# Optimization experiments

Hardware: AMD Instinct MI355X
Metric: run time of the kernel (lower is better)

Reference implementation:

```python
import jax, jax.numpy as jnp
import numpy as np

B, T, U, V, H, KA, KO = 64, 600, 64, 80, 512, 10, 20


def setup_inputs() -> dict:
    key = jax.random.key(0)
    ks = jax.random.split(key, 12)
    std = 0.075
    p = lambda k, shape: jax.random.normal(k, shape, jnp.float32) * std
    return dict(
        char_seq=jax.random.randint(ks[0], (B, U), 0, V),
        char_mask=jnp.ones((B, U), jnp.float32),
        strokes=jax.random.normal(ks[1], (B, T, 3), jnp.float32),
        strokes_mask=jnp.ones((B, T), jnp.float32),
        lstm0_Wih=p(ks[2], (4 * H, 3 + V)), lstm0_Whh=p(ks[3], (4 * H, H)), lstm0_b=jnp.zeros((4 * H,), jnp.float32),
        win_W=p(ks[4], (3 * KA, H)), win_b=jnp.zeros((3 * KA,), jnp.float32),
        lstm1_Wih=p(ks[5], (4 * H, 3 + V + H)), lstm1_Whh=p(ks[6], (4 * H, H)), lstm1_b=jnp.zeros((4 * H,), jnp.float32),
        lstm2_Wih=p(ks[7], (4 * H, 3 + V + H)), lstm2_Whh=p(ks[8], (4 * H, H)), lstm2_b=jnp.zeros((4 * H,), jnp.float32),
        fc_W=p(ks[9], (6 * KO + 1, 3 * H)), fc_b=jnp.zeros((6 * KO + 1,), jnp.float32),
    )


def _lstm_cell(gates_x, h, c, Whh):
    # gates_x already contains x@Wih.T + b; PyTorch gate order: i, f, g, o
    gates = gates_x + h @ Whh.T
    i, f, g, o = jnp.split(gates, 4, axis=-1)
    c = jax.nn.sigmoid(f) * c + jax.nn.sigmoid(i) * jnp.tanh(g)
    h = jax.nn.sigmoid(o) * jnp.tanh(c)
    return h, c


def _run_lstm(x, Wih, Whh, b):
    # x: [B, T, F]; precompute input projection once (big GEMM), scan only on h.
    gx = jnp.einsum('btf,gf->btg', x, Wih) + b  # [B,T,4H]
    h0 = jnp.zeros((x.shape[0], H), x.dtype)
    c0 = jnp.zeros((x.shape[0], H), x.dtype)

    def step(carry, g_t):
        h, c = carry
        h, c = _lstm_cell(g_t, h, c, Whh)
        return (h, c), h

    _, hs = jax.lax.scan(step, (h0, c0), gx.transpose(1, 0, 2))
    return hs.transpose(1, 0, 2)  # [B,T,H]


def _forward(char_seq, char_mask, strokes,
             lstm0_Wih, lstm0_Whh, lstm0_b, win_W, win_b,
             lstm1_Wih, lstm1_Whh, lstm1_b, lstm2_Wih, lstm2_Whh, lstm2_b,
             fc_W, fc_b):
    char_oh = jax.nn.one_hot(char_seq, V, dtype=jnp.float32) * char_mask[..., None]  # [B,U,V]
    u_grid = jnp.arange(U, dtype=jnp.float32)  # char positions

    h0 = jnp.zeros((B, H), jnp.float32)
    c0 = jnp.zeros((B, H), jnp.float32)
    w0 = jnp.zeros((B, V), jnp.float32)
    k0 = jnp.zeros((B, KA), jnp.float32)

    def step(carry, x_t):
        h, c, w, k = carry
        inp = jnp.concatenate([x_t, w], axis=-1)  # [B, 3+V]
        gates = inp @ lstm0_Wih.T + lstm0_b
        h, c = _lstm_cell(gates, h, c, lstm0_Whh)
        # Gaussian attention window (Graves 2013)
        p = h @ win_W.T + win_b  # [B, 3K]
        alpha, beta, kap_hat = jnp.split(jnp.exp(p), 3, axis=-1)
        k = k + kap_hat  # [B,K]
        phi = jnp.sum(alpha[:, :, None] * jnp.exp(-beta[:, :, None] * (k[:, :, None] - u_grid) ** 2), axis=1)
        phi = phi * char_mask  # [B,U]
        w = jnp.einsum('bu,buv->bv', phi, char_oh)
        return (h, c, w, k), (h, w)

    _, (h_seq, w_seq) = jax.lax.scan(step, (h0, c0, w0, k0), strokes.transpose(1, 0, 2))
    lstm0_out = h_seq.transpose(1, 0, 2)   # [B,T,H]
    attn_out = w_seq.transpose(1, 0, 2)    # [B,T,V]

    lstm1_out = _run_lstm(jnp.concatenate([strokes, attn_out, lstm0_out], -1), lstm1_Wih, lstm1_Whh, lstm1_b)
    lstm2_out = _run_lstm(jnp.concatenate([strokes, attn_out, lstm1_out], -1), lstm2_Wih, lstm2_Whh, lstm2_b)

    final = jnp.einsum('bth,gh->btg', jnp.concatenate([lstm0_out, lstm1_out, lstm2_out], -1), fc_W) + fc_b
    # parse_outputs: split [2K, 2K, K, K, 1]
    myu = final[..., : 2 * KO]
    log_sigma = final[..., 2 * KO: 4 * KO]
    pi = final[..., 4 * KO: 5 * KO]
    rho = final[..., 5 * KO: 6 * KO]
    eos = final[..., 6 * KO:]
    log_pi = jax.nn.log_softmax(pi, axis=-1)
    rho = jnp.tanh(rho)
    eos = jax.nn.sigmoid(-eos)
    myu = myu.reshape(myu.shape[:-1] + (KO, 2))
    log_sigma = log_sigma.reshape(log_sigma.shape[:-1] + (KO, 2))
    return (log_pi, myu, log_sigma, rho, eos)


def reference(char_seq, char_mask, strokes, strokes_mask,
              lstm0_Wih, lstm0_Whh, lstm0_b, win_W, win_b,
              lstm1_Wih, lstm1_Whh, lstm1_b, lstm2_Wih, lstm2_Whh, lstm2_b,
              fc_W, fc_b):
    # strokes_mask is unused by forward() in the original module (only in losses)
    return _forward(char_seq, char_mask, strokes,
                    lstm0_Wih, lstm0_Whh, lstm0_b, win_W, win_b,
                    lstm1_Wih, lstm1_Whh, lstm1_b, lstm2_Wih, lstm2_Whh, lstm2_b,
                    fc_W, fc_b)
```

## Files before the change

kernel.cpp:

```cpp
#include <hip/hip_runtime.h>
#include <math.h>

#define B_ 64
#define T_ 600
#define U_ 64
#define V_ 80
#define H_ 512
#define KA_ 10
#define KO_ 20

#define S0_ 600
#define S12_ 1108
#define NLB_ 64
#define NWB_ 64

typedef unsigned u32x4 __attribute__((ext_vector_type(4)));

__device__ __forceinline__ float sigmf(float x){ return 1.0f/(1.0f+expf(-x)); }

__device__ __forceinline__ int coh_load_i32(const int* p){
    int v;
    asm volatile("global_load_dword %0, %1, off sc0 sc1\n\ts_waitcnt vmcnt(0)"
                 : "=v"(v) : "v"(p) : "memory");
    return v;
}
__device__ __forceinline__ void coh_store_u32(unsigned* p, unsigned v){
    asm volatile("global_store_dword %0, %1, off sc0 sc1" :: "v"(p), "v"(v) : "memory");
}
__device__ __forceinline__ void coh_store_u128(unsigned* p, u32x4 v){
    asm volatile("global_store_dwordx4 %0, %1, off sc0 sc1" :: "v"(p), "v"(v) : "memory");
}
__device__ __forceinline__ void spin_ge(int* p, int target){
    while (coh_load_i32(p) < target) __builtin_amdgcn_s_sleep(1);
}
#define BLOCK_WAIT(p, tgt) do { if (threadIdx.x == 0) spin_ge((p), (tgt)); __syncthreads(); } while (0)

__device__ __forceinline__ float blo(unsigned u){ return __uint_as_float(u << 16); }
__device__ __forceinline__ float bhi(unsigned u){ return __uint_as_float(u & 0xffff0000u); }
__device__ __forceinline__ unsigned pack_bf16(float a, float b){
    return ((__float_as_uint(a) + 0x8000u) >> 16) | ((__float_as_uint(b) + 0x8000u) & 0xffff0000u);
}

__global__ __launch_bounds__(64) void k_prep(
    const float* __restrict__ W0ih, const float* __restrict__ W0hh,
    const float* __restrict__ W1ih, const float* __restrict__ W1hh,
    const float* __restrict__ W2ih, const float* __restrict__ W2hh,
    float* __restrict__ wpad)
{
    int r = blockIdx.x;
    int tid = threadIdx.x;
    if (r < 2048){
        float* dst = wpad + (size_t)r*S0_;
        const float* sih = W0ih + (size_t)r*83;
        const float* shh = W0hh + (size_t)r*512;
        if (tid < 3) dst[tid] = sih[tid];
        if (tid == 3) dst[3] = 0.f;
        for (int v=tid; v<V_; v+=64) dst[4+v] = sih[3+v];
        for (int k=tid; k<H_; k+=64) dst[84+k] = shh[k];
    } else {
        int rr = r - 2048;
        int layer = rr >> 11;
        int row = rr & 2047;
        const float* sih = (layer==0 ? W1ih : W2ih) + (size_t)row*595;
        const float* shh = (layer==0 ? W1hh : W2hh) + (size_t)row*512;
        float* dst = wpad + (size_t)2048*S0_ + ((size_t)layer*2048 + row)*S12_;
        if (tid < 3) dst[tid] = sih[tid];
        if (tid == 3) dst[3] = 0.f;
        for (int v=tid; v<V_; v+=64) dst[4+v] = sih[3+v];
        for (int k=tid; k<H_; k+=64) dst[84+k] = sih[83+k];
        for (int k=tid; k<H_; k+=64) dst[596+k] = shh[k];
    }
}

#define FMA8(W, OFF) do { \
    float4 qa = *(const float4*)((W) + (OFF)); \
    float4 qb = *(const float4*)((W) + (OFF) + 4); \
    A0 += x0*qa.x + x1*qa.y + x2*qa.z + x3*qa.w + x4*qb.x + x5*qb.y + x6*qb.z + x7*qb.w; \
} while (0)

__global__ __launch_bounds__(512, 2) void k_pipe(
    const float* __restrict__ strokes,
    const int*   __restrict__ char_seq,
    const float* __restrict__ char_mask,
    const float* __restrict__ wpad,
    const float* __restrict__ winW, const float* __restrict__ winb,
    const float* __restrict__ b0, const float* __restrict__ b1, const float* __restrict__ b2,
    unsigned* __restrict__ out0b, unsigned* __restrict__ out1b, unsigned* __restrict__ out2b,
    unsigned* __restrict__ attnb, int* __restrict__ sync)
{
    __builtin_amdgcn_fence(__ATOMIC_ACQUIRE, "agent");

    int* c0 = sync;
    int* c1 = sync + 640;
    int* c2 = sync + 1280;
    int* cw = sync + 1920;

    const int bid = blockIdx.x;
    const int tid = threadIdx.x;
    const int b   = tid & 63;
    const int r   = tid >> 6;

    __shared__ float sh[8][64];
    __shared__ float shh[512];
    __shared__ float pp[30][16];
    __shared__ float sa[KA_], sbv[KA_], sk[KA_], skst[KA_];
    __shared__ float sphi[U_];
    __shared__ float satt[V_];
    __shared__ int   sseq[U_];
    __shared__ float smask[U_];

    if (bid >= 192){
        const int wb = bid - 192;
        if (tid < U_){ sseq[tid] = char_seq[wb*U_+tid]; smask[tid] = char_mask[wb*U_+tid]; }
        __syncthreads();
        for (int t=0; t<T_; ++t){
            BLOCK_WAIT(&c0[t], NLB_);
            if (tid < 64){
                uint4 q = ((const uint4*)out0b)[((size_t)t*64 + tid)*64 + wb];
                shh[8*tid+0]=blo(q.x); shh[8*tid+1]=bhi(q.x);
                shh[8*tid+2]=blo(q.y); shh[8*tid+3]=bhi(q.y);
                shh[8*tid+4]=blo(q.z); shh[8*tid+5]=bhi(q.z);
                shh[8*tid+6]=blo(q.w); shh[8*tid+7]=bhi(q.w);
            }
            __syncthreads();
            if (tid < 480){
                int rr = tid >> 4, p = tid & 15;
                const float* wrow = winW + (size_t)rr*H_;
                float acc = 0.f;
                #pragma unroll 8
                for (int i=0; i<32; ++i) acc += shh[p+16*i]*wrow[p+16*i];
                pp[rr][p] = acc;
            }
            __syncthreads();
            if (tid < 30){
                float pv = winb[tid];
                #pragma unroll
                for (int i=0; i<16; ++i) pv += pp[tid][i];
                float e = expf(pv);
                if (tid < KA_) sa[tid] = e;
                else if (tid < 2*KA_) sbv[tid-KA_] = e;
                else {
                    int a2 = tid - 2*KA_;
                    float kn = ((t == 0) ? 0.f : skst[a2]) + e;
                    skst[a2] = kn; sk[a2] = kn;
                }
            }
            __syncthreads();
            if (tid < U_){
                float acc = 0.f;
                #pragma unroll
                for (int a=0; a<KA_; ++a){
                    float d = sk[a] - (float)tid;
                    acc += sa[a]*expf(-sbv[a]*d*d);
                }
                sphi[tid] = acc * smask[tid]*smask[tid];
            }
            __syncthreads();
            if (tid < V_){
                float wv = 0.f;
                for (int u=0; u<U_; ++u) wv += (sseq[u] == tid) ? sphi[u] : 0.f;
                satt[tid] = wv;
            }
            __syncthreads();
            if (tid < 40){
                coh_store_u32(attnb + (size_t)t*2560 + (size_t)wb*40 + tid,
                              pack_bf16(satt[2*tid], satt[2*tid+1]));
                asm volatile("s_waitcnt vmcnt(0)" ::: "memory");
            }
            __syncthreads();
            if (tid == 0) atomicAdd(&cw[t], 1);
        }
        return;
    }

    const int l  = bid >> 6;
    const int ub = (bid & 63) * 8;
    const int cu = ub + r;

    const float* wbase; const float* bias_p; size_t wst;
    unsigned* hbo; const unsigned* hbp; int* cself; int* cprev;
    if (l == 0){ wbase = wpad;                                  wst = S0_;  bias_p = b0; hbo = out0b; hbp = nullptr; cself = c0; cprev = nullptr; }
    else if (l == 1){ wbase = wpad + (size_t)2048*S0_;          wst = S12_; bias_p = b1; hbo = out1b; hbp = out0b;  cself = c1; cprev = c0; }
    else { wbase = wpad + (size_t)2048*S0_ + (size_t)2048*S12_; wst = S12_; bias_p = b2; hbo = out2b; hbp = out1b;  cself = c2; cprev = c1; }

    const float* w0 = wbase + (size_t)(0*H_+cu)*wst;
    const float* w1 = wbase + (size_t)(1*H_+cu)*wst;
    const float* w2 = wbase + (size_t)(2*H_+cu)*wst;
    const float* w3 = wbase + (size_t)(3*H_+cu)*wst;

    const float bq0 = bias_p[0*H_+cu];
    const float bq1 = bias_p[1*H_+cu];
    const float bq2 = bias_p[2*H_+cu];
    const float bq3 = bias_p[3*H_+cu];
    float creg = 0.f;

    for (int t=0; t<T_; ++t){
        float a0, a1, a2, a3;
        {
            const float* sr = strokes + ((size_t)b*T_ + t)*3;
            float sx=sr[0], sy=sr[1], sz=sr[2];
            a0 = sx*w0[0] + sy*w0[1] + sz*w0[2];
            a1 = sx*w1[0] + sy*w1[1] + sz*w1[2];
            a2 = sx*w2[0] + sy*w2[1] + sz*w2[2];
            a3 = sx*w3[0] + sy*w3[1] + sz*w3[2];
        }

        if (l == 0){
            if (t > 0){
                BLOCK_WAIT(&c0[t-1], NLB_);
                const uint4* hp = (const uint4*)out0b + (size_t)(t-1)*4096 + b;
                #pragma unroll 4
                for (int kp=0; kp<64; ++kp){
                    uint4 q = hp[(size_t)kp*64];
                    float x0=blo(q.x),x1=bhi(q.x),x2=blo(q.y),x3=bhi(q.y);
                    float x4=blo(q.z),x5=bhi(q.z),x6=blo(q.w),x7=bhi(q.w);
                    int o = 84 + 8*kp;
                    { float A0=a0; FMA8(w0,o); a0=A0; }
                    { float A0=a1; FMA8(w1,o); a1=A0; }
                    { float A0=a2; FMA8(w2,o); a2=A0; }
                    { float A0=a3; FMA8(w3,o); a3=A0; }
                }
                BLOCK_WAIT(&cw[t-1], NWB_);
                const uint4* ap = (const uint4*)(attnb + (size_t)(t-1)*2560 + (size_t)b*40);
                #pragma unroll
                for (int j=0; j<10; ++j){
                    uint4 q = ap[j];
                    float x0=blo(q.x),x1=bhi(q.x),x2=blo(q.y),x3=bhi(q.y);
                    float x4=blo(q.z),x5=bhi(q.z),x6=blo(q.w),x7=bhi(q.w);
                    int o = 4 + 8*j;
                    { float A0=a0; FMA8(w0,o); a0=A0; }
                    { float A0=a1; FMA8(w1,o); a1=A0; }
                    { float A0=a2; FMA8(w2,o); a2=A0; }
                    { float A0=a3; FMA8(w3,o); a3=A0; }
                }
            }
        } else {
            if (tid == 0){
                if (t > 0) spin_ge(&cself[t-1], NLB_);
                spin_ge(&cprev[t], NLB_);
                spin_ge(&cw[t], NWB_);
            }
            __syncthreads();
            const uint4* hc = (const uint4*)hbp + (size_t)t*4096 + b;
            if (t > 0){
                const uint4* ho = (const uint4*)hbo + (size_t)(t-1)*4096 + b;
                #pragma unroll 2
                for (int kp=0; kp<64; ++kp){
                    uint4 qo = ho[(size_t)kp*64];
                    uint4 qc = hc[(size_t)kp*64];
                    {
                        float x0=blo(qo.x),x1=bhi(qo.x),x2=blo(qo.y),x3=bhi(qo.y);
                        float x4=blo(qo.z),x5=bhi(qo.z),x6=blo(qo.w),x7=bhi(qo.w);
                        int o = 596 + 8*kp;
                        { float A0=a0; FMA8(w0,o); a0=A0; }
                        { float A0=a1; FMA8(w1,o); a1=A0; }
                        { float A0=a2; FMA8(w2,o); a2=A0; }
                        { float A0=a3; FMA8(w3,o); a3=A0; }
                    }
                    {
                        float x0=blo(qc.x),x1=bhi(qc.x),x2=blo(qc.y),x3=bhi(qc.y);
                        float x4=blo(qc.z),x5=bhi(qc.z),x6=blo(qc.w),x7=bhi(qc.w);
                        int o = 84 + 8*kp;
                        { float A0=a0; FMA8(w0,o); a0=A0; }
                        { float A0=a1; FMA8(w1,o); a1=A0; }
                        { float A0=a2; FMA8(w2,o); a2=A0; }
                        { float A0=a3; FMA8(w3,o); a3=A0; }
                    }
                }
            } else {
                #pragma unroll 4
                for (int kp=0; kp<64; ++kp){
                    uint4 qc = hc[(size_t)kp*64];
                    float x0=blo(qc.x),x1=bhi(qc.x),x2=blo(qc.y),x3=bhi(qc.y);
                    float x4=blo(qc.z),x5=bhi(qc.z),x6=blo(qc.w),x7=bhi(qc.w);
                    int o = 84 + 8*kp;
                    { float A0=a0; FMA8(w0,o); a0=A0; }
                    { float A0=a1; FMA8(w1,o); a1=A0; }
                    { float A0=a2; FMA8(w2,o); a2=A0; }
                    { float A0=a3; FMA8(w3,o); a3=A0; }
                }
            }
            const uint4* ap = (const uint4*)(attnb + (size_t)t*2560 + (size_t)b*40);
            #pragma unroll
            for (int j=0; j<10; ++j){
                uint4 q = ap[j];
                float x0=blo(q.x),x1=bhi(q.x),x2=blo(q.y),x3=bhi(q.y);
                float x4=blo(q.z),x5=bhi(q.z),x6=blo(q.w),x7=bhi(q.w);
                int o = 4 + 8*j;
                { float A0=a0; FMA8(w0,o); a0=A0; }
                { float A0=a1; FMA8(w1,o); a1=A0; }
                { float A0=a2; FMA8(w2,o); a2=A0; }
                { float A0=a3; FMA8(w3,o); a3=A0; }
            }
        }

        {
            float gi  = a0 + bq0;
            float gf  = a1 + bq1;
            float gg_ = a2 + bq2;
            float go  = a3 + bq3;
            float cold = (t == 0) ? 0.f : creg;
            float cnew = sigmf(gf)*cold + sigmf(gi)*tanhf(gg_);
            creg = cnew;
            sh[r][b] = sigmf(go)*tanhf(cnew);
        }
        __syncthreads();
        if (tid < 64){
            u32x4 v;
            v.x = pack_bf16(sh[0][tid], sh[1][tid]);
            v.y = pack_bf16(sh[2][tid], sh[3][tid]);
            v.z = pack_bf16(sh[4][tid], sh[5][tid]);
            v.w = pack_bf16(sh[6][tid], sh[7][tid]);
            coh_store_u128(hbo + (size_t)t*16384 + (size_t)(ub>>3)*256 + tid*4, v);
            asm volatile("s_waitcnt vmcnt(0)" ::: "memory");
        }
        __syncthreads();
        if (tid == 0) atomicAdd(&cself[t], 1);
    }
}

__global__ __launch_bounds__(256) void k_fc(
    const unsigned* __restrict__ out0b, const unsigned* __restrict__ out1b, const unsigned* __restrict__ out2b,
    const float* __restrict__ fcW, const float* __restrict__ fcb, float* __restrict__ out)
{
    int t = blockIdx.x; int tid = threadIdx.x;
    int b = tid & 63; int gq = tid >> 6;
    __shared__ float smraw[128*65];

    float acc[31];
    #pragma unroll
    for (int i=0; i<31; ++i) acc[i] = 0.f;

    const unsigned* hbs[3] = {out0b, out1b, out2b};
    for (int seg=0; seg<3; ++seg){
        const uint4* o = (const uint4*)hbs[seg];
        for (int kc=0; kc<H_; kc+=128){
            int kp0 = kc >> 3;
            __syncthreads();
            #pragma unroll
            for (int rr=0; rr<4; ++rr){
                int idx = tid + 256*rr;
                int kq  = idx >> 6;
                int bb  = idx & 63;
                uint4 v = o[((size_t)t*64 + kp0 + kq)*64 + bb];
                int kb = kq*8;
                smraw[(kb+0)*65+bb]=blo(v.x); smraw[(kb+1)*65+bb]=bhi(v.x);
                smraw[(kb+2)*65+bb]=blo(v.y); smraw[(kb+3)*65+bb]=bhi(v.y);
                smraw[(kb+4)*65+bb]=blo(v.z); smraw[(kb+5)*65+bb]=bhi(v.z);
                smraw[(kb+6)*65+bb]=blo(v.w); smraw[(kb+7)*65+bb]=bhi(v.w);
            }
            __syncthreads();
            for (int kk=0; kk<128; kk+=4){
                float a0 = smraw[(kk+0)*65+b];
                float a1 = smraw[(kk+1)*65+b];
                float a2 = smraw[(kk+2)*65+b];
                float a3 = smraw[(kk+3)*65+b];
                int K = seg*H_ + kc + kk;
                #pragma unroll
                for (int i=0; i<30; ++i){
                    float4 w = *(const float4*)(fcW + (size_t)(gq+4*i)*1536 + K);
                    acc[i] += a0*w.x + a1*w.y + a2*w.z + a3*w.w;
                }
                if (gq == 0){
                    float4 w = *(const float4*)(fcW + (size_t)120*1536 + K);
                    acc[30] += a0*w.x + a1*w.y + a2*w.z + a3*w.w;
                }
            }
        }
    }
    __syncthreads();
    #pragma unroll
    for (int i=0; i<30; ++i) smraw[(gq+4*i)*64 + b] = acc[i] + fcb[gq+4*i];
    if (gq == 0) smraw[120*64 + b] = acc[30] + fcb[120];
    __syncthreads();

    if (tid < 64){
        size_t bt = (size_t)b*T_ + t;
        float* myu = out + 768000;
        #pragma unroll
        for (int q=0; q<10; ++q){
            float4 v;
            v.x = smraw[(4*q+0)*64+b]; v.y = smraw[(4*q+1)*64+b];
            v.z = smraw[(4*q+2)*64+b]; v.w = smraw[(4*q+3)*64+b];
            *(float4*)(myu + bt*40 + 4*q) = v;
        }
        float* lsg = out + 2304000;
        #pragma unroll
        for (int q=0; q<10; ++q){
            float4 v;
            v.x = smraw[(40+4*q+0)*64+b]; v.y = smraw[(40+4*q+1)*64+b];
            v.z = smraw[(40+4*q+2)*64+b]; v.w = smraw[(40+4*q+3)*64+b];
            *(float4*)(lsg + bt*40 + 4*q) = v;
        }
        float pi[KO_];
        float m = -1e30f;
        #pragma unroll
        for (int ko=0; ko<KO_; ++ko){ pi[ko] = smraw[(80+ko)*64+b]; m = fmaxf(m, pi[ko]); }
        float s = 0.f;
        #pragma unroll
        for (int ko=0; ko<KO_; ++ko) s += expf(pi[ko]-m);
        float lse = m + logf(s);
        #pragma unroll
        for (int q=0; q<5; ++q){
            float4 v;
            v.x = pi[4*q+0]-lse; v.y = pi[4*q+1]-lse; v.z = pi[4*q+2]-lse; v.w = pi[4*q+3]-lse;
            *(float4*)(out + bt*20 + 4*q) = v;
        }
        float* rho = out + 3840000;
        #pragma unroll
        for (int q=0; q<5; ++q){
            float4 v;
            v.x = tanhf(smraw[(100+4*q+0)*64+b]); v.y = tanhf(smraw[(100+4*q+1)*64+b]);
            v.z = tanhf(smraw[(100+4*q+2)*64+b]); v.w = tanhf(smraw[(100+4*q+3)*64+b]);
            *(float4*)(rho + bt*20 + 4*q) = v;
        }
        out[4608000 + bt] = 1.f/(1.f + expf(smraw[120*64+b]));
    }
}

extern "C" void kernel_launch(void* const* d_in, const int* in_sizes, int n_in,
                              void* d_out, int out_size, void* d_ws, size_t ws_size,
                              hipStream_t stream)
{
    const int*   char_seq  = (const int*)  d_in[0];
    const float* char_mask = (const float*)d_in[1];
    const float* strokes   = (const float*)d_in[2];
    const float* W0ih = (const float*)d_in[4];
    const float* W0hh = (const float*)d_in[5];
    const float* b0   = (const float*)d_in[6];
    const float* winW = (const float*)d_in[7];
    const float* winb = (const float*)d_in[8];
    const float* W1ih = (const float*)d_in[9];
    const float* W1hh = (const float*)d_in[10];
    const float* b1   = (const float*)d_in[11];
    const float* W2ih = (const float*)d_in[12];
    const float* W2hh = (const float*)d_in[13];
    const float* b2   = (const float*)d_in[14];
    const float* fcW  = (const float*)d_in[15];
    const float* fcb  = (const float*)d_in[16];

    unsigned* out0b = (unsigned*)d_ws;
    unsigned* out1b = out0b + 9830400;
    unsigned* out2b = out1b + 9830400;
    unsigned* attnb = out2b + 9830400;
    float*    wpad  = (float*)(attnb + 1536000);
    int*      sync  = (int*)(wpad + 5767168);

    (void)hipMemsetAsync(sync, 0, 2560*sizeof(int), stream);

    hipLaunchKernelGGL(k_prep, dim3(6144), dim3(64), 0, stream,
        W0ih, W0hh, W1ih, W1hh, W2ih, W2hh, wpad);

    hipLaunchKernelGGL(k_pipe, dim3(256), dim3(512), 0, stream,
        strokes, char_seq, char_mask, wpad, winW, winb, b0, b1, b2,
        out0b, out1b, out2b, attnb, sync);

    hipLaunchKernelGGL(k_fc, dim3(600), dim3(256), 0, stream,
        out0b, out1b, out2b, fcW, fcb, (float*)d_out);
}
```

Before: 54.57 ms.

## Keep fp16 LSTM weights resident in LDS, use fdot2, replace atomic counters with per-block flags

Recurrent and input weights are packed to fp16 in the prep kernel. Each persistent block loads its 32 gate rows into dynamic shared memory once and reuses them for all 600 steps, instead of streaming fp32 weights from global or L2 every step. Dot products use the packed fp16 dot instruction, and the activations are exchanged as fp16 rather than bf16. Cross-block synchronisation switches from atomicAdd counters to per-block padded flags that 64 threads poll in parallel. This cuts per-step memory traffic and atomic latency, at the cost of fp16 precision and about 71KB of LDS per block, which may limit occupancy.

```diff
diff --git a/kernel.cpp b/kernel.cpp
--- a/kernel.cpp
+++ b/kernel.cpp
@@ -9,99 +9,124 @@
 #define KA_ 10
 #define KO_ 20
 
-#define S0_ 600
-#define S12_ 1108
-#define NLB_ 64
-#define NWB_ 64
+#define RW0   300
+#define RW12  556
+#define WOFF1 614400
+#define WOFF2 1753088
+#define WOFFW 2891776
+#define FSTRIDE 16
 
 typedef unsigned u32x4 __attribute__((ext_vector_type(4)));
+typedef _Float16 h2_t __attribute__((ext_vector_type(2)));
 
 __device__ __forceinline__ float sigmf(float x){ return 1.0f/(1.0f+expf(-x)); }
 
-__device__ __forceinline__ int coh_load_i32(const int* p){
-    int v;
+static __device__ __forceinline__ h2_t bch(unsigned u){ return __builtin_bit_cast(h2_t, u); }
+static __device__ __forceinline__ unsigned pkh(float a, float b){
+    return __builtin_bit_cast(unsigned, __builtin_amdgcn_cvt_pkrtz(a, b));
+}
+static __device__ __forceinline__ float hlo(unsigned u){ return (float)bch(u)[0]; }
+static __device__ __forceinline__ float hhi(unsigned u){ return (float)bch(u)[1]; }
+
+#if __has_builtin(__builtin_amdgcn_fdot2)
+static __device__ __forceinline__ float fd2(unsigned a, unsigned b, float c){
+    return __builtin_amdgcn_fdot2(bch(a), bch(b), c, false);
+}
+#else
+static __device__ __forceinline__ float fd2(unsigned a, unsigned b, float c){
+    return c + hlo(a)*hlo(b) + hhi(a)*hhi(b);
+}
+#endif
+
+static __device__ __forceinline__ float dot8(uint4 q, uint4 w, float acc){
+    acc = fd2(q.x, w.x, acc);
+    acc = fd2(q.y, w.y, acc);
+    acc = fd2(q.z, w.z, acc);
+    acc = fd2(q.w, w.w, acc);
+    return acc;
+}
+
+static __device__ __forceinline__ unsigned coh_load_u32(const unsigned* p){
+    unsigned v;
     asm volatile("global_load_dword %0, %1, off sc0 sc1\n\ts_waitcnt vmcnt(0)"
                  : "=v"(v) : "v"(p) : "memory");
     return v;
 }
-__device__ __forceinline__ void coh_store_u32(unsigned* p, unsigned v){
+static __device__ __forceinline__ void coh_store_u32(unsigned* p, unsigned v){
     asm volatile("global_store_dword %0, %1, off sc0 sc1" :: "v"(p), "v"(v) : "memory");
 }
-__device__ __forceinline__ void coh_store_u128(unsigned* p, u32x4 v){
+static __device__ __forceinline__ void coh_store_u128(unsigned* p, u32x4 v){
     asm volatile("global_store_dwordx4 %0, %1, off sc0 sc1" :: "v"(p), "v"(v) : "memory");
 }
-__device__ __forceinline__ void spin_ge(int* p, int target){
-    while (coh_load_i32(p) < target) __builtin_amdgcn_s_sleep(1);
-}
-#define BLOCK_WAIT(p, tgt) do { if (threadIdx.x == 0) spin_ge((p), (tgt)); __syncthreads(); } while (0)
-
-__device__ __forceinline__ float blo(unsigned u){ return __uint_as_float(u << 16); }
-__device__ __forceinline__ float bhi(unsigned u){ return __uint_as_float(u & 0xffff0000u); }
-__device__ __forceinline__ unsigned pack_bf16(float a, float b){
-    return ((__float_as_uint(a) + 0x8000u) >> 16) | ((__float_as_uint(b) + 0x8000u) & 0xffff0000u);
+static __device__ __forceinline__ void wait_role(const unsigned* f){
+    if (threadIdx.x < 64){
+        const unsigned* p = f + threadIdx.x*FSTRIDE;
+        while (coh_load_u32(p) == 0){}
+    }
+    __syncthreads();
 }
 
 __global__ __launch_bounds__(64) void k_prep(
     const float* __restrict__ W0ih, const float* __restrict__ W0hh,
     const float* __restrict__ W1ih, const float* __restrict__ W1hh,
     const float* __restrict__ W2ih, const float* __restrict__ W2hh,
-    float* __restrict__ wpad)
+    const float* __restrict__ winW,
+    unsigned* __restrict__ wpad32)
 {
-    int r = blockIdx.x;
-    int tid = threadIdx.x;
-    if (r < 2048){
-        float* dst = wpad + (size_t)r*S0_;
-        const float* sih = W0ih + (size_t)r*83;
-        const float* shh = W0hh + (size_t)r*512;
-        if (tid < 3) dst[tid] = sih[tid];
-        if (tid == 3) dst[3] = 0.f;
-        for (int v=tid; v<V_; v+=64) dst[4+v] = sih[3+v];
-        for (int k=tid; k<H_; k+=64) dst[84+k] = shh[k];
+    int r = blockIdx.x; int tid = threadIdx.x;
+    if (r < 6144){
+        int layer = r >> 11;
+        int row = r & 2047;
+        const float* ih; const float* hh; unsigned* dst; int RW;
+        if (layer == 0){ ih = W0ih + (size_t)row*83;  hh = W0hh + (size_t)row*512; dst = wpad32 + (size_t)row*RW0;           RW = RW0; }
+        else if (layer == 1){ ih = W1ih + (size_t)row*595; hh = W1hh + (size_t)row*512; dst = wpad32 + WOFF1 + (size_t)row*RW12; RW = RW12; }
+        else { ih = W2ih + (size_t)row*595; hh = W2hh + (size_t)row*512; dst = wpad32 + WOFF2 + (size_t)row*RW12; RW = RW12; }
+        for (int j = tid; j < RW; j += 64){
+            float f[2];
+            #pragma unroll
+            for (int q = 0; q < 2; ++q){
+                int e = 2*j + q;
+                float v = 0.f;
+                if (e < 3) v = ih[e];
+                else if (e >= 8 && e < 88) v = ih[3 + e - 8];
+                else if (e >= 88 && e < 600) v = (layer == 0) ? hh[e-88] : ih[83 + e - 88];
+                else if (e >= 600 && e < 1112 && layer != 0) v = hh[e-600];
+                f[q] = v;
+            }
+            dst[j] = pkh(f[0], f[1]);
+        }
     } else {
-        int rr = r - 2048;
-        int layer = rr >> 11;
-        int row = rr & 2047;
-        const float* sih = (layer==0 ? W1ih : W2ih) + (size_t)row*595;
-        const float* shh = (layer==0 ? W1hh : W2hh) + (size_t)row*512;
-        float* dst = wpad + (size_t)2048*S0_ + ((size_t)layer*2048 + row)*S12_;
-        if (tid < 3) dst[tid] = sih[tid];
-        if (tid == 3) dst[3] = 0.f;
-        for (int v=tid; v<V_; v+=64) dst[4+v] = sih[3+v];
-        for (int k=tid; k<H_; k+=64) dst[84+k] = sih[83+k];
-        for (int k=tid; k<H_; k+=64) dst[596+k] = shh[k];
-    }
-}
-
-#define FMA8(W, OFF) do { \
-    float4 qa = *(const float4*)((W) + (OFF)); \
-    float4 qb = *(const float4*)((W) + (OFF) + 4); \
-    A0 += x0*qa.x + x1*qa.y + x2*qa.z + x3*qa.w + x4*qb.x + x5*qb.y + x6*qb.z + x7*qb.w; \
-} while (0)
+        int rr = r - 6144;
+        unsigned* dst = wpad32 + WOFFW + (size_t)rr*256;
+        const float* src = winW + (size_t)rr*512;
+        for (int j = tid; j < 256; j += 64)
+            dst[j] = pkh(src[2*j], src[2*j+1]);
+    }
+}
 
 __global__ __launch_bounds__(512, 2) void k_pipe(
     const float* __restrict__ strokes,
     const int*   __restrict__ char_seq,
     const float* __restrict__ char_mask,
-    const float* __restrict__ wpad,
-    const float* __restrict__ winW, const float* __restrict__ winb,
+    const unsigned* __restrict__ wpad32,
+    const float* __restrict__ winb,
     const float* __restrict__ b0, const float* __restrict__ b1, const float* __restrict__ b2,
     unsigned* __restrict__ out0b, unsigned* __restrict__ out1b, unsigned* __restrict__ out2b,
-    unsigned* __restrict__ attnb, int* __restrict__ sync)
+    unsigned* __restrict__ attnb, unsigned* __restrict__ flags)
 {
     __builtin_amdgcn_fence(__ATOMIC_ACQUIRE, "agent");
 
-    int* c0 = sync;
-    int* c1 = sync + 640;
-    int* c2 = sync + 1280;
-    int* cw = sync + 1920;
+    unsigned* cf0 = flags;
+    unsigned* cf1 = flags + 614400;
+    unsigned* cf2 = flags + 1228800;
+    unsigned* cfw = flags + 1843200;
 
     const int bid = blockIdx.x;
     const int tid = threadIdx.x;
     const int b   = tid & 63;
     const int r   = tid >> 6;
 
-    __shared__ float sh[8][64];
-    __shared__ float shh[512];
+    extern __shared__ unsigned dynls[];
     __shared__ float pp[30][16];
     __shared__ float sa[KA_], sbv[KA_], sk[KA_], skst[KA_];
     __shared__ float sphi[U_];
@@ -111,31 +136,29 @@
 
     if (bid >= 192){
         const int wb = bid - 192;
+        unsigned* wlw = dynls;
+        unsigned* shh = dynls + 7680;
+        for (int i = tid; i < 7680; i += 512) wlw[i] = wpad32[WOFFW + i];
         if (tid < U_){ sseq[tid] = char_seq[wb*U_+tid]; smask[tid] = char_mask[wb*U_+tid]; }
         __syncthreads();
-        for (int t=0; t<T_; ++t){
-            BLOCK_WAIT(&c0[t], NLB_);
-            if (tid < 64){
-                uint4 q = ((const uint4*)out0b)[((size_t)t*64 + tid)*64 + wb];
-                shh[8*tid+0]=blo(q.x); shh[8*tid+1]=bhi(q.x);
-                shh[8*tid+2]=blo(q.y); shh[8*tid+3]=bhi(q.y);
-                shh[8*tid+4]=blo(q.z); shh[8*tid+5]=bhi(q.z);
-                shh[8*tid+6]=blo(q.w); shh[8*tid+7]=bhi(q.w);
-            }
+        for (int t = 0; t < T_; ++t){
+            wait_role(cf0 + (size_t)t*1024);
+            if (tid < 64)
+                ((uint4*)shh)[tid] = ((const uint4*)out0b)[((size_t)t*64 + tid)*64 + wb];
             __syncthreads();
             if (tid < 480){
                 int rr = tid >> 4, p = tid & 15;
-                const float* wrow = winW + (size_t)rr*H_;
+                const unsigned* wr = wlw + rr*256;
                 float acc = 0.f;
-                #pragma unroll 8
-                for (int i=0; i<32; ++i) acc += shh[p+16*i]*wrow[p+16*i];
+                #pragma unroll
+                for (int i = 0; i < 16; ++i){ int j = p + 16*i; acc = fd2(shh[j], wr[j], acc); }
                 pp[rr][p] = acc;
             }
             __syncthreads();
             if (tid < 30){
                 float pv = winb[tid];
                 #pragma unroll
-                for (int i=0; i<16; ++i) pv += pp[tid][i];
+                for (int i = 0; i < 16; ++i) pv += pp[tid][i];
                 float e = expf(pv);
                 if (tid < KA_) sa[tid] = e;
                 else if (tid < 2*KA_) sbv[tid-KA_] = e;
@@ -149,7 +172,7 @@
             if (tid < U_){
                 float acc = 0.f;
                 #pragma unroll
-                for (int a=0; a<KA_; ++a){
+                for (int a = 0; a < KA_; ++a){
                     float d = sk[a] - (float)tid;
                     acc += sa[a]*expf(-sbv[a]*d*d);
                 }
@@ -158,139 +181,134 @@
             __syncthreads();
             if (tid < V_){
                 float wv = 0.f;
-                for (int u=0; u<U_; ++u) wv += (sseq[u] == tid) ? sphi[u] : 0.f;
+                for (int u = 0; u < U_; ++u) wv += (sseq[u] == tid) ? sphi[u] : 0.f;
                 satt[tid] = wv;
             }
             __syncthreads();
             if (tid < 40){
                 coh_store_u32(attnb + (size_t)t*2560 + (size_t)wb*40 + tid,
-                              pack_bf16(satt[2*tid], satt[2*tid+1]));
+                              pkh(satt[2*tid], satt[2*tid+1]));
                 asm volatile("s_waitcnt vmcnt(0)" ::: "memory");
-            }
-            __syncthreads();
-            if (tid == 0) atomicAdd(&cw[t], 1);
+                if (tid == 0) coh_store_u32(cfw + (size_t)t*1024 + wb*FSTRIDE, 1u);
+            }
         }
         return;
     }
 
-    const int l  = bid >> 6;
-    const int ub = (bid & 63) * 8;
-    const int cu = ub + r;
-
-    const float* wbase; const float* bias_p; size_t wst;
-    unsigned* hbo; const unsigned* hbp; int* cself; int* cprev;
-    if (l == 0){ wbase = wpad;                                  wst = S0_;  bias_p = b0; hbo = out0b; hbp = nullptr; cself = c0; cprev = nullptr; }
-    else if (l == 1){ wbase = wpad + (size_t)2048*S0_;          wst = S12_; bias_p = b1; hbo = out1b; hbp = out0b;  cself = c1; cprev = c0; }
-    else { wbase = wpad + (size_t)2048*S0_ + (size_t)2048*S12_; wst = S12_; bias_p = b2; hbo = out2b; hbp = out1b;  cself = c2; cprev = c1; }
-
-    const float* w0 = wbase + (size_t)(0*H_+cu)*wst;
-    const float* w1 = wbase + (size_t)(1*H_+cu)*wst;
-    const float* w2 = wbase + (size_t)(2*H_+cu)*wst;
-    const float* w3 = wbase + (size_t)(3*H_+cu)*wst;
-
+    const int l   = bid >> 6;
+    const int blk = bid & 63;
+    const int ub  = blk * 8;
+    const int cu  = ub + r;
+
+    const unsigned* wsrc; int RW;
+    const float* bias_p; unsigned* hbo; const unsigned* hbp;
+    unsigned* cfself; const unsigned* cfprev;
+    if (l == 0){ wsrc = wpad32;          RW = RW0;  bias_p = b0; hbo = out0b; hbp = nullptr; cfself = cf0; cfprev = nullptr; }
+    else if (l == 1){ wsrc = wpad32 + WOFF1; RW = RW12; bias_p = b1; hbo = out1b; hbp = out0b; cfself = cf1; cfprev = cf0; }
+    else { wsrc = wpad32 + WOFF2; RW = RW12; bias_p = b2; hbo = out2b; hbp = out1b; cfself = cf2; cfprev = cf1; }
+
+    unsigned* wl = dynls;
+    float* shf = (float*)(dynls + 32*RW);
+    for (int i = tid; i < 32*RW; i += 512){
+        int row = i / RW, j = i - row*RW;
+        int ul = row >> 2, g = row & 3;
+        wl[i] = wsrc[(size_t)(g*H_ + ub + ul)*RW + j];
+    }
+    __syncthreads();
+
+    const uint4* Wr0 = (const uint4*)(wl + (size_t)(r*4+0)*RW);
+    const uint4* Wr1 = (const uint4*)(wl + (size_t)(r*4+1)*RW);
+    const uint4* Wr2 = (const uint4*)(wl + (size_t)(r*4+2)*RW);
+    const uint4* Wr3 = (const uint4*)(wl + (size_t)(r*4+3)*RW);
+
+    float stw[4][3];
+    #pragma unroll
+    for (int g = 0; g < 4; ++g){
+        unsigned wa = wl[(size_t)(r*4+g)*RW + 0];
+        unsigned wb2 = wl[(size_t)(r*4+g)*RW + 1];
+        stw[g][0] = hlo(wa); stw[g][1] = hhi(wa); stw[g][2] = hlo(wb2);
+    }
     const float bq0 = bias_p[0*H_+cu];
     const float bq1 = bias_p[1*H_+cu];
     const float bq2 = bias_p[2*H_+cu];
     const float bq3 = bias_p[3*H_+cu];
     float creg = 0.f;
 
-    for (int t=0; t<T_; ++t){
-        float a0, a1, a2, a3;
-        {
-            const float* sr = strokes + ((size_t)b*T_ + t)*3;
-            float sx=sr[0], sy=sr[1], sz=sr[2];
-            a0 = sx*w0[0] + sy*w0[1] + sz*w0[2];
-            a1 = sx*w1[0] + sy*w1[1] + sz*w1[2];
-            a2 = sx*w2[0] + sy*w2[1] + sz*w2[2];
-            a3 = sx*w3[0] + sy*w3[1] + sz*w3[2];
-        }
+    for (int t = 0; t < T_; ++t){
+        const float* sr = strokes + ((size_t)b*T_ + t)*3;
+        float sx = sr[0], sy = sr[1], sz = sr[2];
+        float a0 = sx*stw[0][0] + sy*stw[0][1] + sz*stw[0][2];
+        float a1 = sx*stw[1][0] + sy*stw[1][1] + sz*stw[1][2];
+        float a2 = sx*stw[2][0] + sy*stw[2][1] + sz*stw[2][2];
+        float a3 = sx*stw[3][0] + sy*stw[3][1] + sz*stw[3][2];
 
         if (l == 0){
             if (t > 0){
-                BLOCK_WAIT(&c0[t-1], NLB_);
-                const uint4* hp = (const uint4*)out0b + (size_t)(t-1)*4096 + b;
+                wait_role(cf0 + (size_t)(t-1)*1024);
+                const uint4* hq = (const uint4*)hbo + (size_t)(t-1)*4096 + b;
                 #pragma unroll 4
-                for (int kp=0; kp<64; ++kp){
-                    uint4 q = hp[(size_t)kp*64];
-                    float x0=blo(q.x),x1=bhi(q.x),x2=blo(q.y),x3=bhi(q.y);
-                    float x4=blo(q.z),x5=bhi(q.z),x6=blo(q.w),x7=bhi(q.w);
-                    int o = 84 + 8*kp;
-                    { float A0=a0; FMA8(w0,o); a0=A0; }
-                    { float A0=a1; FMA8(w1,o); a1=A0; }
-                    { float A0=a2; FMA8(w2,o); a2=A0; }
-                    { float A0=a3; FMA8(w3,o); a3=A0; }
-                }
-                BLOCK_WAIT(&cw[t-1], NWB_);
+                for (int kp = 0; kp < 64; ++kp){
+                    uint4 q = hq[(size_t)kp*64];
+                    a0 = dot8(q, Wr0[11+kp], a0);
+                    a1 = dot8(q, Wr1[11+kp], a1);
+                    a2 = dot8(q, Wr2[11+kp], a2);
+                    a3 = dot8(q, Wr3[11+kp], a3);
+                }
+                wait_role(cfw + (size_t)(t-1)*1024);
                 const uint4* ap = (const uint4*)(attnb + (size_t)(t-1)*2560 + (size_t)b*40);
                 #pragma unroll
-                for (int j=0; j<10; ++j){
+                for (int j = 0; j < 10; ++j){
                     uint4 q = ap[j];
-                    float x0=blo(q.x),x1=bhi(q.x),x2=blo(q.y),x3=bhi(q.y);
-                    float x4=blo(q.z),x5=bhi(q.z),x6=blo(q.w),x7=bhi(q.w);
-                    int o = 4 + 8*j;
-                    { float A0=a0; FMA8(w0,o); a0=A0; }
-                    { float A0=a1; FMA8(w1,o); a1=A0; }
-                    { float A0=a2; FMA8(w2,o); a2=A0; }
-                    { float A0=a3; FMA8(w3,o); a3=A0; }
+                    a0 = dot8(q, Wr0[1+j], a0);
+                    a1 = dot8(q, Wr1[1+j], a1);
+                    a2 = dot8(q, Wr2[1+j], a2);
+                    a3 = dot8(q, Wr3[1+j], a3);
                 }
             }
         } else {
-            if (tid == 0){
-                if (t > 0) spin_ge(&cself[t-1], NLB_);
-                spin_ge(&cprev[t], NLB_);
-                spin_ge(&cw[t], NWB_);
+            if (tid < 64){
+                if (t > 0){
+                    const unsigned* p = cfself + (size_t)(t-1)*1024 + tid*FSTRIDE;
+                    while (coh_load_u32(p) == 0){}
+                }
+            } else if (tid < 128){
+                const unsigned* p = cfprev + (size_t)t*1024 + (tid-64)*FSTRIDE;
+                while (coh_load_u32(p) == 0){}
+            } else if (tid < 192){
+                const unsigned* p = cfw + (size_t)t*1024 + (tid-128)*FSTRIDE;
+                while (coh_load_u32(p) == 0){}
             }
             __syncthreads();
             const uint4* hc = (const uint4*)hbp + (size_t)t*4096 + b;
             if (t > 0){
                 const uint4* ho = (const uint4*)hbo + (size_t)(t-1)*4096 + b;
                 #pragma unroll 2
-                for (int kp=0; kp<64; ++kp){
+                for (int kp = 0; kp < 64; ++kp){
                     uint4 qo = ho[(size_t)kp*64];
                     uint4 qc = hc[(size_t)kp*64];
-                    {
-                        float x0=blo(qo.x),x1=bhi(qo.x),x2=blo(qo.y),x3=bhi(qo.y);
-                        float x4=blo(qo.z),x5=bhi(qo.z),x6=blo(qo.w),x7=bhi(qo.w);
-                        int o = 596 + 8*kp;
-                        { float A0=a0; FMA8(w0,o); a0=A0; }
-                        { float A0=a1; FMA8(w1,o); a1=A0; }
-                        { float A0=a2; FMA8(w2,o); a2=A0; }
-                        { float A0=a3; FMA8(w3,o); a3=A0; }
-                    }
-                    {
-                        float x0=blo(qc.x),x1=bhi(qc.x),x2=blo(qc.y),x3=bhi(qc.y);
-                        float x4=blo(qc.z),x5=bhi(qc.z),x6=blo(qc.w),x7=bhi(qc.w);
-                        int o = 84 + 8*kp;
-                        { float A0=a0; FMA8(w0,o); a0=A0; }
-                        { float A0=a1; FMA8(w1,o); a1=A0; }
-                        { float A0=a2; FMA8(w2,o); a2=A0; }
-                        { float A0=a3; FMA8(w3,o); a3=A0; }
-                    }
+                    a0 = dot8(qo, Wr0[75+kp], a0); a0 = dot8(qc, Wr0[11+kp], a0);
+                    a1 = dot8(qo, Wr1[75+kp], a1); a1 = dot8(qc, Wr1[11+kp], a1);
+                    a2 = dot8(qo, Wr2[75+kp], a2); a2 = dot8(qc, Wr2[11+kp], a2);
+                    a3 = dot8(qo, Wr3[75+kp], a3); a3 = dot8(qc, Wr3[11+kp], a3);
                 }
             } else {
                 #pragma unroll 4
-                for (int kp=0; kp<64; ++kp){
+                for (int kp = 0; kp < 64; ++kp){
                     uint4 qc = hc[(size_t)kp*64];
-                    float x0=blo(qc.x),x1=bhi(qc.x),x2=blo(qc.y),x3=bhi(qc.y);
-                    float x4=blo(qc.z),x5=bhi(qc.z),x6=blo(qc.w),x7=bhi(qc.w);
-                    int o = 84 + 8*kp;
-                    { float A0=a0; FMA8(w0,o); a0=A0; }
-                    { float A0=a1; FMA8(w1,o); a1=A0; }
-                    { float A0=a2; FMA8(w2,o); a2=A0; }
-                    { float A0=a3; FMA8(w3,o); a3=A0; }
+                    a0 = dot8(qc, Wr0[11+kp], a0);
+                    a1 = dot8(qc, Wr1[11+kp], a1);
+                    a2 = dot8(qc, Wr2[11+kp], a2);
+                    a3 = dot8(qc, Wr3[11+kp], a3);
                 }
             }
             const uint4* ap = (const uint4*)(attnb + (size_t)t*2560 + (size_t)b*40);
             #pragma unroll
-            for (int j=0; j<10; ++j){
+            for (int j = 0; j < 10; ++j){
                 uint4 q = ap[j];
-                float x0=blo(q.x),x1=bhi(q.x),x2=blo(q.y),x3=bhi(q.y);
-                float x4=blo(q.z),x5=bhi(q.z),x6=blo(q.w),x7=bhi(q.w);
-                int o = 4 + 8*j;
-                { float A0=a0; FMA8(w0,o); a0=A0; }
-                { float A0=a1; FMA8(w1,o); a1=A0; }
-                { float A0=a2; FMA8(w2,o); a2=A0; }
-                { float A0=a3; FMA8(w3,o); a3=A0; }
+                a0 = dot8(q, Wr0[1+j], a0);
+                a1 = dot8(q, Wr1[1+j], a1);
+                a2 = dot8(q, Wr2[1+j], a2);
+                a3 = dot8(q, Wr3[1+j], a3);
             }
         }
 
@@ -302,20 +320,19 @@
             float cold = (t == 0) ? 0.f : creg;
             float cnew = sigmf(gf)*cold + sigmf(gi)*tanhf(gg_);
             creg = cnew;
-            sh[r][b] = sigmf(go)*tanhf(cnew);
+            shf[r*64 + b] = sigmf(go)*tanhf(cnew);
         }
         __syncthreads();
         if (tid < 64){
             u32x4 v;
-            v.x = pack_bf16(sh[0][tid], sh[1][tid]);
-            v.y = pack_bf16(sh[2][tid], sh[3][tid]);
-            v.z = pack_bf16(sh[4][tid], sh[5][tid]);
-            v.w = pack_bf16(sh[6][tid], sh[7][tid]);
-            coh_store_u128(hbo + (size_t)t*16384 + (size_t)(ub>>3)*256 + tid*4, v);
+            v.x = pkh(shf[0*64+tid], shf[1*64+tid]);
+            v.y = pkh(shf[2*64+tid], shf[3*64+tid]);
+            v.z = pkh(shf[4*64+tid], shf[5*64+tid]);
+            v.w = pkh(shf[6*64+tid], shf[7*64+tid]);
+            coh_store_u128(hbo + (size_t)t*16384 + (size_t)blk*256 + tid*4, v);
             asm volatile("s_waitcnt vmcnt(0)" ::: "memory");
-        }
-        __syncthreads();
-        if (tid == 0) atomicAdd(&cself[t], 1);
+            if (tid == 0) coh_store_u32(cfself + (size_t)t*1024 + blk*FSTRIDE, 1u);
+        }
     }
 }
 
@@ -329,35 +346,35 @@
 
     float acc[31];
     #pragma unroll
-    for (int i=0; i<31; ++i) acc[i] = 0.f;
+    for (int i = 0; i < 31; ++i) acc[i] = 0.f;
 
     const unsigned* hbs[3] = {out0b, out1b, out2b};
-    for (int seg=0; seg<3; ++seg){
+    for (int seg = 0; seg < 3; ++seg){
         const uint4* o = (const uint4*)hbs[seg];
-        for (int kc=0; kc<H_; kc+=128){
+        for (int kc = 0; kc < H_; kc += 128){
             int kp0 = kc >> 3;
             __syncthreads();
             #pragma unroll
-            for (int rr=0; rr<4; ++rr){
+            for (int rr = 0; rr < 4; ++rr){
                 int idx = tid + 256*rr;
                 int kq  = idx >> 6;
                 int bb  = idx & 63;
                 uint4 v = o[((size_t)t*64 + kp0 + kq)*64 + bb];
                 int kb = kq*8;
-                smraw[(kb+0)*65+bb]=blo(v.x); smraw[(kb+1)*65+bb]=bhi(v.x);
-                smraw[(kb+2)*65+bb]=blo(v.y); smraw[(kb+3)*65+bb]=bhi(v.y);
-                smraw[(kb+4)*65+bb]=blo(v.z); smraw[(kb+5)*65+bb]=bhi(v.z);
-                smraw[(kb+6)*65+bb]=blo(v.w); smraw[(kb+7)*65+bb]=bhi(v.w);
-            }
-            __syncthreads();
-            for (int kk=0; kk<128; kk+=4){
+                smraw[(kb+0)*65+bb]=hlo(v.x); smraw[(kb+1)*65+bb]=hhi(v.x);
+                smraw[(kb+2)*65+bb]=hlo(v.y); smraw[(kb+3)*65+bb]=hhi(v.y);
+                smraw[(kb+4)*65+bb]=hlo(v.z); smraw[(kb+5)*65+bb]=hhi(v.z);
+                smraw[(kb+6)*65+bb]=hlo(v.w); smraw[(kb+7)*65+bb]=hhi(v.w);
+            }
+            __syncthreads();
+            for (int kk = 0; kk < 128; kk += 4){
                 float a0 = smraw[(kk+0)*65+b];
                 float a1 = smraw[(kk+1)*65+b];
                 float a2 = smraw[(kk+2)*65+b];
                 float a3 = smraw[(kk+3)*65+b];
                 int K = seg*H_ + kc + kk;
                 #pragma unroll
-                for (int i=0; i<30; ++i){
+                for (int i = 0; i < 30; ++i){
                     float4 w = *(const float4*)(fcW + (size_t)(gq+4*i)*1536 + K);
                     acc[i] += a0*w.x + a1*w.y + a2*w.z + a3*w.w;
                 }
@@ -370,7 +387,7 @@
     }
     __syncthreads();
     #pragma unroll
-    for (int i=0; i<30; ++i) smraw[(gq+4*i)*64 + b] = acc[i] + fcb[gq+4*i];
+    for (int i = 0; i < 30; ++i) smraw[(gq+4*i)*64 + b] = acc[i] + fcb[gq+4*i];
     if (gq == 0) smraw[120*64 + b] = acc[30] + fcb[120];
     __syncthreads();
 
@@ -378,7 +395,7 @@
         size_t bt = (size_t)b*T_ + t;
         float* myu = out + 768000;
         #pragma unroll
-        for (int q=0; q<10; ++q){
+        for (int q = 0; q < 10; ++q){
             float4 v;
             v.x = smraw[(4*q+0)*64+b]; v.y = smraw[(4*q+1)*64+b];
             v.z = smraw[(4*q+2)*64+b]; v.w = smraw[(4*q+3)*64+b];
@@ -386,7 +403,7 @@
         }
         float* lsg = out + 2304000;
         #pragma unroll
-        for (int q=0; q<10; ++q){
+        for (int q = 0; q < 10; ++q){
             float4 v;
             v.x = smraw[(40+4*q+0)*64+b]; v.y = smraw[(40+4*q+1)*64+b];
             v.z = smraw[(40+4*q+2)*64+b]; v.w = smraw[(40+4*q+3)*64+b];
@@ -395,20 +412,20 @@
         float pi[KO_];
         float m = -1e30f;
         #pragma unroll
-        for (int ko=0; ko<KO_; ++ko){ pi[ko] = smraw[(80+ko)*64+b]; m = fmaxf(m, pi[ko]); }
+        for (int ko = 0; ko < KO_; ++ko){ pi[ko] = smraw[(80+ko)*64+b]; m = fmaxf(m, pi[ko]); }
         float s = 0.f;
         #pragma unroll
-        for (int ko=0; ko<KO_; ++ko) s += expf(pi[ko]-m);
+        for (int ko = 0; ko < KO_; ++ko) s += expf(pi[ko]-m);
         float lse = m + logf(s);
         #pragma unroll
-        for (int q=0; q<5; ++q){
+        for (int q = 0; q < 5; ++q){
             float4 v;
             v.x = pi[4*q+0]-lse; v.y = pi[4*q+1]-lse; v.z = pi[4*q+2]-lse; v.w = pi[4*q+3]-lse;
             *(float4*)(out + bt*20 + 4*q) = v;
         }
         float* rho = out + 3840000;
         #pragma unroll
-        for (int q=0; q<5; ++q){
+        for (int q = 0; q < 5; ++q){
             float4 v;
             v.x = tanhf(smraw[(100+4*q+0)*64+b]); v.y = tanhf(smraw[(100+4*q+1)*64+b]);
             v.z = tanhf(smraw[(100+4*q+2)*64+b]); v.w = tanhf(smraw[(100+4*q+3)*64+b]);
@@ -439,21 +456,25 @@
     const float* fcW  = (const float*)d_in[15];
     const float* fcb  = (const float*)d_in[16];
 
-    unsigned* out0b = (unsigned*)d_ws;
-    unsigned* out1b = out0b + 9830400;
-    unsigned* out2b = out1b + 9830400;
-    unsigned* attnb = out2b + 9830400;
-    float*    wpad  = (float*)(attnb + 1536000);
-    int*      sync  = (int*)(wpad + 5767168);
-
-    (void)hipMemsetAsync(sync, 0, 2560*sizeof(int), stream);
-
-    hipLaunchKernelGGL(k_prep, dim3(6144), dim3(64), 0, stream,
-        W0ih, W0hh, W1ih, W1hh, W2ih, W2hh, wpad);
-
-    hipLaunchKernelGGL(k_pipe, dim3(256), dim3(512), 0, stream,
-        strokes, char_seq, char_mask, wpad, winW, winb, b0, b1, b2,
-        out0b, out1b, out2b, attnb, sync);
+    unsigned* out0b  = (unsigned*)d_ws;
+    unsigned* out1b  = out0b + 9830400;
+    unsigned* out2b  = out1b + 9830400;
+    unsigned* attnb  = out2b + 9830400;
+    unsigned* wpad32 = attnb + 1536000;
+    unsigned* flags  = wpad32 + 2899456;
+
+    (void)hipMemsetAsync(flags, 0, 2457600u*sizeof(unsigned), stream);
+
+    hipLaunchKernelGGL(k_prep, dim3(6174), dim3(64), 0, stream,
+        W0ih, W0hh, W1ih, W1hh, W2ih, W2hh, winW, wpad32);
+
+    const int dyn_bytes = (32*RW12 + 512) * 4;
+    (void)hipFuncSetAttribute((const void*)k_pipe,
+        hipFuncAttributeMaxDynamicSharedMemorySize, dyn_bytes);
+
+    hipLaunchKernelGGL(k_pipe, dim3(256), dim3(512), dyn_bytes, stream,
+        strokes, char_seq, char_mask, wpad32, winb, b0, b1, b2,
+        out0b, out1b, out2b, attnb, flags);
 
     hipLaunchKernelGGL(k_fc, dim3(600), dim3(256), 0, stream,
         out0b, out1b, out2b, fcW, fcb, (float*)d_out);
```

Result: slower. 76.62 ms (+40.4%).
